# Performance work log

Measured on AMD Instinct MI355X. Metric: run time of the kernel, lower is better.

## Reference

```python
import jax, jax.numpy as jnp
import numpy as np

D_MODEL = 128
D_STATE = 16
D_CONV = 2
EXPAND = 2
D_INNER = EXPAND * D_MODEL  # 256
DT_RANK = (D_MODEL + 15) // 16  # 8
GROUPS = 4
EPS = 1e-5


def setup_inputs() -> dict:
    key = jax.random.key(0)
    ks = jax.random.split(key, 12)
    s = lambda k, shape, sc=0.02: jax.random.normal(k, shape, dtype=jnp.float32) * sc
    inp = {
        "x_hsi": jax.random.normal(ks[0], (8, D_MODEL, 64, 64), dtype=jnp.float32),
        "W_in": s(ks[1], (D_MODEL, 2 * D_INNER)),            # in_proj (no bias)
        "conv_w": s(ks[2], (D_INNER, D_CONV), 0.5),          # depthwise causal conv, k=2
        "conv_b": s(ks[3], (D_INNER,), 0.1),
        "W_x": s(ks[4], (D_INNER, DT_RANK + 2 * D_STATE)),   # x_proj (no bias)
        "W_dt": s(ks[5], (DT_RANK, D_INNER), 0.1),
        "b_dt": s(ks[6], (D_INNER,), 0.1),
        "A_log": jnp.log(jnp.broadcast_to(jnp.arange(1, D_STATE + 1, dtype=jnp.float32), (D_INNER, D_STATE))),
        "D": jnp.ones((D_INNER,), dtype=jnp.float32),
        "W_out": s(ks[7], (D_INNER, D_MODEL)),               # out_proj (no bias)
        "gn_gamma": jnp.ones((D_MODEL,), dtype=jnp.float32),
        "gn_beta": jnp.zeros((D_MODEL,), dtype=jnp.float32),
    }
    return inp


def _causal_conv_k2(x, w, b):
    # x: [B, L, Din]; w: [Din, 2]; causal depthwise conv, kernel size 2
    xp = jnp.pad(x, ((0, 0), (1, 0), (0, 0)))
    return xp[:, :-1] * w[:, 0] + xp[:, 1:] * w[:, 1] + b


def _selective_scan(xc, dt, Bmat, Cmat, A, D):
    # xc,dt: [B,L,Din]; Bmat,Cmat: [B,L,N]; A: [Din,N]; D: [Din]
    def step(h, inp):
        dt_t, B_t, C_t, x_t = inp          # [B,Din],[B,N],[B,N],[B,Din]
        dA = jnp.exp(dt_t[..., None] * A)                      # [B,Din,N]
        dBx = dt_t[..., None] * B_t[:, None, :] * x_t[..., None]
        h = dA * h + dBx
        y = jnp.einsum('bdn,bn->bd', h, C_t)
        return h, y

    B_, L, Din = xc.shape
    h0 = jnp.zeros((B_, Din, A.shape[1]), dtype=xc.dtype)
    xs = (jnp.swapaxes(dt, 0, 1), jnp.swapaxes(Bmat, 0, 1),
          jnp.swapaxes(Cmat, 0, 1), jnp.swapaxes(xc, 0, 1))
    _, ys = jax.lax.scan(step, h0, xs)     # ys: [L,B,Din]
    return jnp.swapaxes(ys, 0, 1) + xc * D


def _mamba(x, W_in, conv_w, conv_b, W_x, W_dt, b_dt, A_log, D, W_out):
    # x: [B, L, d_model]
    xz = x @ W_in                                   # [B,L,2*Din]
    xh, z = jnp.split(xz, 2, axis=-1)
    xh = jax.nn.silu(_causal_conv_k2(xh, conv_w, conv_b))
    x_dbl = xh @ W_x                                # [B,L,dt_rank+2N]
    dt_low = x_dbl[..., :DT_RANK]
    Bmat = x_dbl[..., DT_RANK:DT_RANK + D_STATE]
    Cmat = x_dbl[..., DT_RANK + D_STATE:]
    dt = jax.nn.softplus(dt_low @ W_dt + b_dt)      # [B,L,Din]
    A = -jnp.exp(A_log)
    y = _selective_scan(xh, dt, Bmat, Cmat, A, D)
    y = y * jax.nn.silu(z)
    return y @ W_out


def _group_norm(x, gamma, beta):
    # x: [B,C,H,W]
    B_, C, H, W = x.shape
    xr = x.reshape(B_, GROUPS, -1)
    mean = xr.mean(-1, keepdims=True)
    var = xr.var(-1, keepdims=True)
    xn = ((xr - mean) * jax.lax.rsqrt(var + EPS)).reshape(B_, C, H, W)
    return xn * gamma[:, None, None] + beta[:, None, None]


def reference(x_hsi, W_in, conv_w, conv_b, W_x, W_dt, b_dt, A_log, D, W_out, gn_gamma, gn_beta):
    B_, C, H, W = x_hsi.shape
    x = jnp.transpose(x_hsi, (0, 2, 3, 1)).reshape(B_, H * W, C)
    x = _mamba(x, W_in, conv_w, conv_b, W_x, W_dt, b_dt, A_log, D, W_out)
    x = jnp.transpose(x.reshape(B_, H, W, C), (0, 3, 1, 2))
    x = jax.nn.silu(_group_norm(x, gn_gamma, gn_beta))
    return x + x_hsi
```

## Files before the change

kernel.cpp:

```cpp
#include <hip/hip_runtime.h>
#include <hip/hip_bf16.h>
#include <hip/hip_fp16.h>
#include <math.h>

#define BATCH   8
#define LSEQ    4096
#define CMODEL  128
#define DIN     256
#define NSTATE  16
#define RRANK   8
#define NCH     128
#define TCH     32

typedef __attribute__((ext_vector_type(8))) short short8;
typedef __attribute__((ext_vector_type(4))) float f32x4;
typedef __attribute__((ext_vector_type(2))) float f32x2;

__device__ __forceinline__ float sigmoid_fast(float x) {
    return __builtin_amdgcn_rcpf(1.0f + __expf(-x));
}
__device__ __forceinline__ float silu_fast(float x) { return x * sigmoid_fast(x); }
__device__ __forceinline__ float softplus_fast(float x) {
    return fmaxf(x, 0.0f) + __logf(1.0f + __expf(-fabsf(x)));
}
__device__ __forceinline__ float bf2f(unsigned short u) {
    return __uint_as_float(((unsigned)u) << 16);
}
__device__ __forceinline__ unsigned pk2bf(float a, float b) {
    __hip_bfloat162 t = __float22bfloat162_rn(make_float2(a, b));
    unsigned r;
    __builtin_memcpy(&r, &t, 4);
    return r;
}
__device__ __forceinline__ unsigned short f2bf1(float v) {
    return (unsigned short)pk2bf(v, v);
}

__device__ __forceinline__ void dA_powers2(float dtv, const float* A, bool fast,
                                           f32x2* dA2)
{
    if (fast) {
        float e1 = __expf(dtv * A[0]);
        float e2 = e1 * e1;
        dA2[0] = (f32x2){e1, e2};
        f32x2 e2s = (f32x2){e2, e2};
        #pragma unroll
        for (int j = 1; j < 8; ++j) dA2[j] = dA2[j-1] * e2s;
    } else {
        #pragma unroll
        for (int j = 0; j < 8; ++j)
            dA2[j] = (f32x2){__expf(dtv * A[2*j]), __expf(dtv * A[2*j+1])};
    }
}

#define LSTR 72
#define YSTR 264

__device__ __forceinline__ void tr64_bf(const float* __restrict__ src, int lds,
                                        int r0, int c0,
                                        unsigned short* __restrict__ dst, int ldd)
{
    __shared__ float ts[64][65];
    const int tid = threadIdx.x;
    #pragma unroll
    for (int it = 0; it < 4; ++it) {
        int slot = tid + it * 256;
        int i = slot >> 4, j4 = slot & 15;
        float4 v = *(const float4*)&src[(size_t)(r0 + i) * lds + c0 + j4 * 4];
        ts[i][j4*4+0] = v.x; ts[i][j4*4+1] = v.y;
        ts[i][j4*4+2] = v.z; ts[i][j4*4+3] = v.w;
    }
    __syncthreads();
    #pragma unroll
    for (int it = 0; it < 4; ++it) {
        int slot = tid + it * 256;
        int row = slot >> 4, c4 = slot & 15;
        unsigned p0 = pk2bf(ts[c4*4+0][row], ts[c4*4+1][row]);
        unsigned p1 = pk2bf(ts[c4*4+2][row], ts[c4*4+3][row]);
        unsigned long long u = (unsigned long long)p0 | ((unsigned long long)p1 << 32);
        *(unsigned long long*)&dst[(size_t)(c0 + row) * ldd + r0 + c4 * 4] = u;
    }
}

__global__ __launch_bounds__(256) void k0_setup(
    const float* __restrict__ W_in, const float* __restrict__ W_out,
    const float* __restrict__ W_x,
    unsigned short* __restrict__ wtin, unsigned short* __restrict__ wtout,
    unsigned short* __restrict__ wxt, float* __restrict__ part)
{
    const int bid = blockIdx.x;
    if (bid < 16) {
        int ct = bid >> 3, jt = bid & 7;
        tr64_bf(W_in, 512, ct * 64, jt * 64, wtin, 128);
    } else if (bid < 24) {
        int t3 = bid - 16;
        int kt = t3 >> 1, ct = t3 & 1;
        tr64_bf(W_out, 128, kt * 64, ct * 64, wtout, 256);
    } else if (bid == 24) {
        for (int idx = threadIdx.x; idx < 48 * 256; idx += 256) {
            int j = idx >> 8, k = idx & 255;
            float v = (j < 40) ? W_x[k * 40 + j] : 0.0f;
            wxt[(size_t)j * 256 + k] = f2bf1(v);
        }
    } else {
        if (threadIdx.x < 64) part[threadIdx.x] = 0.0f;
    }
}

__global__ __launch_bounds__(512) void k1_gemm_in(
    const float* __restrict__ x_hsi, const unsigned short* __restrict__ wtin,
    unsigned short* __restrict__ xhbf, unsigned short* __restrict__ zbf)
{
    __shared__ __align__(16) unsigned short Abf[128 * LSTR];
    __shared__ __align__(16) unsigned short Bbf[256 * LSTR];
    const int tid = threadIdx.x;
    const int R0  = blockIdx.x * 128;
    const int b   = R0 >> 12;
    const int l0  = R0 & 4095;
    const int jbase = blockIdx.y * 256;

    const int w    = tid >> 6;
    const int lane = tid & 63;
    const int lm   = lane & 15;
    const int q    = lane >> 4;
    const int mbase = (w & 1) * 64;
    const int nbase = (w >> 1) * 64;

    f32x4 acc[4][4];
    #pragma unroll
    for (int i = 0; i < 4; ++i)
        #pragma unroll
        for (int j = 0; j < 4; ++j) acc[i][j] = (f32x4){0.f, 0.f, 0.f, 0.f};

    const int cq = tid & 15;
    const int lq = tid >> 4;

    for (int kc = 0; kc < 128; kc += 64) {
        __syncthreads();
        {
            float v[4][4];
            #pragma unroll
            for (int t = 0; t < 4; ++t) {
                float4 f = *(const float4*)&x_hsi[((b * 128 + kc + cq * 4 + t) << 12) + l0 + lq * 4];
                v[t][0] = f.x; v[t][1] = f.y; v[t][2] = f.z; v[t][3] = f.w;
            }
            #pragma unroll
            for (int i = 0; i < 4; ++i) {
                unsigned p0 = pk2bf(v[0][i], v[1][i]);
                unsigned p1 = pk2bf(v[2][i], v[3][i]);
                unsigned long long u = (unsigned long long)p0 | ((unsigned long long)p1 << 32);
                *(unsigned long long*)&Abf[(lq * 4 + i) * LSTR + cq * 4] = u;
            }
        }
        #pragma unroll
        for (int it = 0; it < 4; ++it) {
            int slot = tid + it * 512;
            int r = slot >> 3, seg = slot & 7;
            short8 vb = *(const short8*)&wtin[(size_t)(jbase + r) * 128 + kc + seg * 8];
            *(short8*)&Bbf[r * LSTR + seg * 8] = vb;
        }
        __syncthreads();
        #pragma unroll
        for (int kt = 0; kt < 2; ++kt) {
            short8 af[4], bfr[4];
            #pragma unroll
            for (int mt = 0; mt < 4; ++mt)
                af[mt] = *(const short8*)&Abf[(mbase + mt * 16 + lm) * LSTR + kt * 32 + q * 8];
            #pragma unroll
            for (int nt = 0; nt < 4; ++nt)
                bfr[nt] = *(const short8*)&Bbf[(nbase + nt * 16 + lm) * LSTR + kt * 32 + q * 8];
            #pragma unroll
            for (int mt = 0; mt < 4; ++mt)
                #pragma unroll
                for (int nt = 0; nt < 4; ++nt)
                    acc[mt][nt] = __builtin_amdgcn_mfma_f32_16x16x32_bf16(
                        af[mt], bfr[nt], acc[mt][nt], 0, 0, 0);
        }
    }

    const bool is_xh = (jbase == 0);
    #pragma unroll
    for (int mt = 0; mt < 4; ++mt) {
        #pragma unroll
        for (int r = 0; r < 4; ++r) {
            int row = R0 + mbase + mt * 16 + q * 4 + r;
            #pragma unroll
            for (int nt = 0; nt < 4; ++nt) {
                int col = nbase + nt * 16 + lm;
                float val = acc[mt][nt][r];
                if (is_xh) xhbf[row * 256 + col] = f2bf1(val);
                else       zbf[row * 256 + col]  = f2bf1(silu_fast(val));
            }
        }
    }
}

__global__ __launch_bounds__(256) void k46_conv_gemm_scan1(
    const unsigned short* __restrict__ xhbf, const float* __restrict__ conv_w,
    const float* __restrict__ conv_b, const unsigned short* __restrict__ wxt,
    const float* __restrict__ W_dt, const float* __restrict__ b_dt,
    const float* __restrict__ A_log,
    float* __restrict__ xdbl, unsigned short* __restrict__ xcbf,
    float* __restrict__ hend, float* __restrict__ dtsg)
{
    __shared__ float cw0[256], cw1[256], cbs[256];
    __shared__ __align__(16) unsigned short xcb[TCH][YSTR];
    __shared__ __align__(16) float xdl[TCH * 40];
    const int tid = threadIdx.x;
    const int chunk = blockIdx.x;
    const int b = blockIdx.y;
    const int R0 = b * LSEQ + chunk * TCH;

    cw0[tid] = conv_w[2 * tid];
    cw1[tid] = conv_w[2 * tid + 1];
    cbs[tid] = conv_b[tid];

    const int d = tid;
    float A[16];
    #pragma unroll
    for (int qq = 0; qq < 4; ++qq) {
        float4 al = *(const float4*)&A_log[d * 16 + qq * 4];
        A[qq*4+0] = -__expf(al.x); A[qq*4+1] = -__expf(al.y);
        A[qq*4+2] = -__expf(al.z); A[qq*4+3] = -__expf(al.w);
    }
    bool fast = true;
    #pragma unroll
    for (int n = 1; n < 16; ++n)
        fast = fast && (fabsf(A[n] - (n + 1) * A[0]) <= 1e-4f * fabsf(A[n]) + 1e-7f);
    float wdt[8];
    #pragma unroll
    for (int r = 0; r < 8; ++r) wdt[r] = W_dt[r * 256 + d];
    const float bdt = b_dt[d];

    __syncthreads();

    #pragma unroll
    for (int it = 0; it < 8; ++it) {
        int idx = tid + it * 256;
        int r = idx >> 6, qq = idx & 63;
        int row = R0 + r;
        int dd = qq * 4;
        ushort4 cu = *(const ushort4*)&xhbf[(size_t)row * 256 + dd];
        float cur[4] = {bf2f(cu.x), bf2f(cu.y), bf2f(cu.z), bf2f(cu.w)};
        float pv[4] = {0.f, 0.f, 0.f, 0.f};
        if ((row & 4095) != 0) {
            ushort4 pu = *(const ushort4*)&xhbf[(size_t)(row - 1) * 256 + dd];
            pv[0] = bf2f(pu.x); pv[1] = bf2f(pu.y);
            pv[2] = bf2f(pu.z); pv[3] = bf2f(pu.w);
        }
        float o[4];
        #pragma unroll
        for (int e = 0; e < 4; ++e)
            o[e] = silu_fast(pv[e] * cw0[dd+e] + cur[e] * cw1[dd+e] + cbs[dd+e]);
        unsigned p0 = pk2bf(o[0], o[1]), p1 = pk2bf(o[2], o[3]);
        unsigned long long u = (unsigned long long)p0 | ((unsigned long long)p1 << 32);
        *(unsigned long long*)&xcb[r][dd] = u;
        *(unsigned long long*)&xcbf[(size_t)row * 256 + dd] = u;
    }
    __syncthreads();

    const int w    = tid >> 6;
    const int lane = tid & 63;
    const int lm   = lane & 15;
    const int q    = lane >> 4;
    {
        const int mt  = w & 1;
        const int nlo = (w < 2) ? 0 : 2;
        const int nn  = (w < 2) ? 2 : 1;
        f32x4 macc[2];
        macc[0] = (f32x4){0.f,0.f,0.f,0.f};
        macc[1] = (f32x4){0.f,0.f,0.f,0.f};
        for (int kc = 0; kc < 256; kc += 32) {
            short8 af = *(const short8*)&xcb[mt * 16 + lm][kc + q * 8];
            #pragma unroll
            for (int t = 0; t < 2; ++t) {
                if (t < nn) {
                    short8 bfr = *(const short8*)&wxt[(size_t)((nlo + t) * 16 + lm) * 256 + kc + q * 8];
                    macc[t] = __builtin_amdgcn_mfma_f32_16x16x32_bf16(
                        af, bfr, macc[t], 0, 0, 0);
                }
            }
        }
        #pragma unroll
        for (int t = 0; t < 2; ++t) {
            if (t < nn) {
                #pragma unroll
                for (int r = 0; r < 4; ++r) {
                    int row = mt * 16 + q * 4 + r;
                    int col = (nlo + t) * 16 + lm;
                    if (col < 40) {
                        float v = macc[t][r];
                        xdl[row * 40 + col] = v;
                        xdbl[(size_t)(R0 + row) * 40 + col] = v;
                    }
                }
            }
        }
    }
    __syncthreads();

    f32x2 h2[8];
    #pragma unroll
    for (int j = 0; j < 8; ++j) h2[j] = (f32x2){0.f, 0.f};
    float dtsum = 0.f;

    #pragma unroll 2
    for (int tt = 0; tt < TCH; ++tt) {
        float xcv = bf2f(xcb[tt][d]);

        float dl[8];
        *(float4*)&dl[0] = *(const float4*)&xdl[tt * 40 + 0];
        *(float4*)&dl[4] = *(const float4*)&xdl[tt * 40 + 4];
        float dtr = bdt;
        #pragma unroll
        for (int r = 0; r < 8; ++r) dtr = fmaf(dl[r], wdt[r], dtr);
        float dtv = softplus_fast(dtr);
        dtsum += dtv;
        float dtx = dtv * xcv;

        float Bv[16];
        *(float4*)&Bv[0]  = *(const float4*)&xdl[tt * 40 + 8];
        *(float4*)&Bv[4]  = *(const float4*)&xdl[tt * 40 + 12];
        *(float4*)&Bv[8]  = *(const float4*)&xdl[tt * 40 + 16];
        *(float4*)&Bv[12] = *(const float4*)&xdl[tt * 40 + 20];

        f32x2 dA2[8];
        dA_powers2(dtv, A, fast, dA2);
        f32x2 dtx2 = (f32x2){dtx, dtx};
        #pragma unroll
        for (int j = 0; j < 8; ++j) {
            f32x2 Bt2 = (f32x2){Bv[2*j], Bv[2*j+1]};
            h2[j] = dA2[j] * h2[j] + dtx2 * Bt2;
        }
    }

    const float* hf = (const float*)h2;
    const int base = ((b * NCH + chunk) * 256 + d) * 16;
    #pragma unroll
    for (int qq = 0; qq < 4; ++qq)
        *(float4*)&hend[base + qq * 4] = make_float4(hf[qq*4], hf[qq*4+1], hf[qq*4+2], hf[qq*4+3]);
    dtsg[(b * NCH + chunk) * 256 + d] = dtsum;
}

__global__ __launch_bounds__(256) void k7_combine(
    const float* __restrict__ dtsg, const float* __restrict__ A_log,
    float* __restrict__ hx)
{
    const int idx = blockIdx.x * 256 + threadIdx.x;
    const int b = idx >> 12;
    const int rem = idx & 4095;
    const int d = rem >> 4, n = rem & 15;
    const float An = -__expf(A_log[d * 16 + n]);
    const int base = b * NCH * 4096 + rem;
    const int sbase = b * NCH * 256 + d;
    float h = 0.f;
    float Sb[8], Eb[8];
    #pragma unroll
    for (int j = 0; j < 8; ++j) {
        Sb[j] = dtsg[sbase + j * 256];
        Eb[j] = hx[base + j * 4096];
    }
    for (int g = 0; g < NCH / 8; ++g) {
        const int o  = base + g * 32768;
        const int so = sbase + g * 2048;
        float Sn[8] = {0,0,0,0,0,0,0,0}, En[8] = {0,0,0,0,0,0,0,0};
        if (g < NCH / 8 - 1) {
            #pragma unroll
            for (int j = 0; j < 8; ++j) {
                Sn[j] = dtsg[so + 2048 + j * 256];
                En[j] = hx[o + 32768 + j * 4096];
            }
        }
        #pragma unroll
        for (int j = 0; j < 8; ++j) {
            hx[o + j * 4096] = h;
            float P = __expf(Sb[j] * An);
            h = fmaf(P, h, Eb[j]);
        }
        #pragma unroll
        for (int j = 0; j < 8; ++j) { Sb[j] = Sn[j]; Eb[j] = En[j]; }
    }
}

__global__ __launch_bounds__(256) void k89_scan2_gemm_out(
    const unsigned short* __restrict__ xcbf, const float* __restrict__ xdbl,
    const float* __restrict__ W_dt, const float* __restrict__ b_dt,
    const float* __restrict__ A_log, const float* __restrict__ Dvec,
    const float* __restrict__ hin, const unsigned short* __restrict__ zbf,
    const unsigned short* __restrict__ wtout,
    unsigned short* __restrict__ out_bf, float* __restrict__ part)
{
    __shared__ __align__(16) unsigned short Ybf[TCH][YSTR];
    __shared__ float pred[8];
    const int tid = threadIdx.x;
    const int chunk = blockIdx.x;
    const int b = blockIdx.y;
    const int t0 = b * LSEQ + chunk * TCH;

    if (tid < 8) pred[tid] = 0.0f;

    const int d = tid;
    float A[16];
    #pragma unroll
    for (int qq = 0; qq < 4; ++qq) {
        float4 al = *(const float4*)&A_log[d * 16 + qq * 4];
        A[qq*4+0] = -__expf(al.x); A[qq*4+1] = -__expf(al.y);
        A[qq*4+2] = -__expf(al.z); A[qq*4+3] = -__expf(al.w);
    }
    bool fast = true;
    #pragma unroll
    for (int n = 1; n < 16; ++n)
        fast = fast && (fabsf(A[n] - (n + 1) * A[0]) <= 1e-4f * fabsf(A[n]) + 1e-7f);
    float wdt[8];
    #pragma unroll
    for (int r = 0; r < 8; ++r) wdt[r] = W_dt[r * 256 + d];
    const float bdt = b_dt[d];
    const float Dd = Dvec[d];

    f32x2 h2[8];
    {
        const int hbase = ((b * NCH + chunk) * 256 + d) * 16;
        float hf[16];
        #pragma unroll
        for (int qq = 0; qq < 4; ++qq) {
            float4 hv = *(const float4*)&hin[hbase + qq * 4];
            hf[qq*4+0] = hv.x; hf[qq*4+1] = hv.y; hf[qq*4+2] = hv.z; hf[qq*4+3] = hv.w;
        }
        #pragma unroll
        for (int j = 0; j < 8; ++j) h2[j] = (f32x2){hf[2*j], hf[2*j+1]};
    }

    #pragma unroll 2
    for (int tt = 0; tt < TCH; ++tt) {
        const int row = t0 + tt;
        const size_t gi = (size_t)row * 256 + d;
        float xcv = bf2f(xcbf[gi]);

        const float* xr = &xdbl[(size_t)row * 40];
        float dl[8], Bv[16], Cv[16];
        *(float4*)&dl[0] = *(const float4*)&xr[0];
        *(float4*)&dl[4] = *(const float4*)&xr[4];
        *(float4*)&Bv[0]  = *(const float4*)&xr[8];
        *(float4*)&Bv[4]  = *(const float4*)&xr[12];
        *(float4*)&Bv[8]  = *(const float4*)&xr[16];
        *(float4*)&Bv[12] = *(const float4*)&xr[20];
        *(float4*)&Cv[0]  = *(const float4*)&xr[24];
        *(float4*)&Cv[4]  = *(const float4*)&xr[28];
        *(float4*)&Cv[8]  = *(const float4*)&xr[32];
        *(float4*)&Cv[12] = *(const float4*)&xr[36];

        float dtr = bdt;
        #pragma unroll
        for (int r = 0; r < 8; ++r) dtr = fmaf(dl[r], wdt[r], dtr);
        float dtv = softplus_fast(dtr);
        float dtx = dtv * xcv;

        f32x2 dA2[8];
        dA_powers2(dtv, A, fast, dA2);
        f32x2 dtx2 = (f32x2){dtx, dtx};
        f32x2 yv2 = (f32x2){0.f, 0.f};
        #pragma unroll
        for (int j = 0; j < 8; ++j) {
            f32x2 Bt2 = (f32x2){Bv[2*j], Bv[2*j+1]};
            f32x2 Ct2 = (f32x2){Cv[2*j], Cv[2*j+1]};
            h2[j] = dA2[j] * h2[j] + dtx2 * Bt2;
            yv2 = yv2 + h2[j] * Ct2;
        }
        float yv = yv2.x + yv2.y;
        yv = fmaf(Dd, xcv, yv);
        Ybf[tt][d] = f2bf1(yv * bf2f(zbf[gi]));
    }
    __syncthreads();

    const int w    = tid >> 6;
    const int lane = tid & 63;
    const int lm   = lane & 15;
    const int q    = lane >> 4;
    const int mbase = (w & 1) * 64;
    const int nbase = (w >> 1) * 16;

    f32x4 acc[4];
    #pragma unroll
    for (int i = 0; i < 4; ++i) acc[i] = (f32x4){0.f, 0.f, 0.f, 0.f};

    for (int ks = 0; ks < 256; ks += 32) {
        short8 bfr = *(const short8*)&Ybf[nbase + lm][ks + q * 8];
        #pragma unroll
        for (int mt = 0; mt < 4; ++mt) {
            short8 af = *(const short8*)&wtout[(size_t)(mbase + mt * 16 + lm) * 256 + ks + q * 8];
            acc[mt] = __builtin_amdgcn_mfma_f32_16x16x32_bf16(
                af, bfr, acc[mt], 0, 0, 0);
        }
    }

    const int l0 = chunk * TCH;
    #pragma unroll
    for (int mt = 0; mt < 4; ++mt) {
        #pragma unroll
        for (int r = 0; r < 4; ++r) {
            int c = mbase + mt * 16 + q * 4 + r;
            long obase = (long)(b * 128 + c) * 4096 + l0;
            out_bf[obase + nbase + lm] = f2bf1(acc[mt][r]);
        }
    }

    float s0 = 0.f, q0 = 0.f, s1 = 0.f, q1 = 0.f;
    #pragma unroll
    for (int mt = 0; mt < 4; ++mt)
        #pragma unroll
        for (int r = 0; r < 4; ++r) {
            float v = acc[mt][r];
            if (mt < 2) { s0 += v; q0 += v * v; }
            else        { s1 += v; q1 += v * v; }
        }
    #pragma unroll
    for (int off = 32; off > 0; off >>= 1) {
        s0 += __shfl_down(s0, off, 64);
        q0 += __shfl_down(q0, off, 64);
        s1 += __shfl_down(s1, off, 64);
        q1 += __shfl_down(q1, off, 64);
    }
    if (lane == 0) {
        int g0 = mbase >> 5;
        atomicAdd(&pred[g0 * 2],           s0);
        atomicAdd(&pred[g0 * 2 + 1],       q0);
        atomicAdd(&pred[(g0 + 1) * 2],     s1);
        atomicAdd(&pred[(g0 + 1) * 2 + 1], q1);
    }
    __syncthreads();
    if (tid < 8) atomicAdd(&part[b * 8 + tid], pred[tid]);
}

__global__ __launch_bounds__(256) void k10c_apply(
    const unsigned short* __restrict__ out_bf, const float* __restrict__ part,
    const float* __restrict__ gamma, const float* __restrict__ beta,
    const float* __restrict__ x_hsi, float* __restrict__ out)
{
    __shared__ float sstat[64];
    if (threadIdx.x < 32) {
        float S = part[threadIdx.x * 2];
        float Q = part[threadIdx.x * 2 + 1];
        const float inv_n = 1.0f / 131072.0f;
        float mean = S * inv_n;
        float var  = Q * inv_n - mean * mean;
        sstat[threadIdx.x * 2]     = mean;
        sstat[threadIdx.x * 2 + 1] = rsqrtf(var + 1e-5f);
    }
    __syncthreads();
    const int idx4 = blockIdx.x * 256 + threadIdx.x;
    const int flat = idx4 * 4;
    const int c = (flat >> 12) & 127;
    const int b = flat >> 19;
    const int g = c >> 5;
    const float mean = sstat[(b * 4 + g) * 2];
    const float inv  = sstat[(b * 4 + g) * 2 + 1];
    const float ga = gamma[c], be = beta[c];
    ushort4 u = *(const ushort4*)&out_bf[flat];
    float4 r = *(const float4*)&x_hsi[flat];
    float vv[4] = {bf2f(u.x), bf2f(u.y), bf2f(u.z), bf2f(u.w)};
    float rr[4] = {r.x, r.y, r.z, r.w};
    float o[4];
    #pragma unroll
    for (int qq = 0; qq < 4; ++qq) {
        float xn = (vv[qq] - mean) * inv;
        float gv = xn * ga + be;
        o[qq] = silu_fast(gv) + rr[qq];
    }
    *(float4*)&out[flat] = make_float4(o[0], o[1], o[2], o[3]);
}

extern "C" void kernel_launch(void* const* d_in, const int* in_sizes, int n_in,
                              void* d_out, int out_size, void* d_ws, size_t ws_size,
                              hipStream_t stream)
{
    const float* x_hsi  = (const float*)d_in[0];
    const float* W_in   = (const float*)d_in[1];
    const float* conv_w = (const float*)d_in[2];
    const float* conv_b = (const float*)d_in[3];
    const float* W_x    = (const float*)d_in[4];
    const float* W_dt   = (const float*)d_in[5];
    const float* b_dt   = (const float*)d_in[6];
    const float* A_log  = (const float*)d_in[7];
    const float* Dv     = (const float*)d_in[8];
    const float* W_out  = (const float*)d_in[9];
    const float* gnw    = (const float*)d_in[10];
    const float* gnb    = (const float*)d_in[11];

    float* ws = (float*)d_ws;
    unsigned short* xhbf = (unsigned short*)(ws + 0);
    unsigned short* zbf  = (unsigned short*)(ws + 4194304);
    float* xdbl   = ws + 8388608;
    float* hx     = ws + 8716288;
    float* dtsg   = ws + 12910592;
    unsigned short* xcbf   = (unsigned short*)(ws + 13172736);
    unsigned short* out_bf = (unsigned short*)(ws + 17367040);
    float* part   = ws + 19464192;
    unsigned short* wtin  = (unsigned short*)(ws + 19464256);
    unsigned short* wtout = (unsigned short*)(ws + 19497024);
    unsigned short* wxt   = (unsigned short*)(ws + 19513408);
    float* outp   = (float*)d_out;

    k0_setup<<<26, 256, 0, stream>>>(W_in, W_out, W_x, wtin, wtout, wxt, part);
    k1_gemm_in<<<dim3(256, 2), 512, 0, stream>>>(x_hsi, wtin, xhbf, zbf);
    k46_conv_gemm_scan1<<<dim3(NCH, BATCH), 256, 0, stream>>>(
        xhbf, conv_w, conv_b, wxt, W_dt, b_dt, A_log, xdbl, xcbf, hx, dtsg);
    k7_combine<<<128, 256, 0, stream>>>(dtsg, A_log, hx);
    k89_scan2_gemm_out<<<dim3(NCH, BATCH), 256, 0, stream>>>(
        xcbf, xdbl, W_dt, b_dt, A_log, Dv, hx, zbf, wtout, out_bf, part);
    k10c_apply<<<4096, 256, 0, stream>>>(out_bf, part, gnw, gnb, x_hsi, outp);
}
```

Measured before the change: 192.1 us.

## Compute local scan output in first pass and apply decaying carry correction later

```diff
diff --git a/kernel.cpp b/kernel.cpp
--- a/kernel.cpp
+++ b/kernel.cpp
@@ -199,8 +199,8 @@
     const unsigned short* __restrict__ xhbf, const float* __restrict__ conv_w,
     const float* __restrict__ conv_b, const unsigned short* __restrict__ wxt,
     const float* __restrict__ W_dt, const float* __restrict__ b_dt,
-    const float* __restrict__ A_log,
-    float* __restrict__ xdbl, unsigned short* __restrict__ xcbf,
+    const float* __restrict__ A_log, const float* __restrict__ Dvec,
+    float* __restrict__ xdbl, __half* __restrict__ ylh,
     float* __restrict__ hend, float* __restrict__ dtsg)
 {
     __shared__ float cw0[256], cw1[256], cbs[256];
@@ -231,6 +231,7 @@
     #pragma unroll
     for (int r = 0; r < 8; ++r) wdt[r] = W_dt[r * 256 + d];
     const float bdt = b_dt[d];
+    const float Dd = Dvec[d];
 
     __syncthreads();
 
@@ -255,7 +256,6 @@
         unsigned p0 = pk2bf(o[0], o[1]), p1 = pk2bf(o[2], o[3]);
         unsigned long long u = (unsigned long long)p0 | ((unsigned long long)p1 << 32);
         *(unsigned long long*)&xcb[r][dd] = u;
-        *(unsigned long long*)&xcbf[(size_t)row * 256 + dd] = u;
     }
     __syncthreads();
 
@@ -318,20 +318,30 @@
         dtsum += dtv;
         float dtx = dtv * xcv;
 
-        float Bv[16];
+        float Bv[16], Cv[16];
         *(float4*)&Bv[0]  = *(const float4*)&xdl[tt * 40 + 8];
         *(float4*)&Bv[4]  = *(const float4*)&xdl[tt * 40 + 12];
         *(float4*)&Bv[8]  = *(const float4*)&xdl[tt * 40 + 16];
         *(float4*)&Bv[12] = *(const float4*)&xdl[tt * 40 + 20];
+        *(float4*)&Cv[0]  = *(const float4*)&xdl[tt * 40 + 24];
+        *(float4*)&Cv[4]  = *(const float4*)&xdl[tt * 40 + 28];
+        *(float4*)&Cv[8]  = *(const float4*)&xdl[tt * 40 + 32];
+        *(float4*)&Cv[12] = *(const float4*)&xdl[tt * 40 + 36];
 
         f32x2 dA2[8];
         dA_powers2(dtv, A, fast, dA2);
         f32x2 dtx2 = (f32x2){dtx, dtx};
+        f32x2 yv2 = (f32x2){0.f, 0.f};
         #pragma unroll
         for (int j = 0; j < 8; ++j) {
             f32x2 Bt2 = (f32x2){Bv[2*j], Bv[2*j+1]};
+            f32x2 Ct2 = (f32x2){Cv[2*j], Cv[2*j+1]};
             h2[j] = dA2[j] * h2[j] + dtx2 * Bt2;
-        }
+            yv2 = yv2 + h2[j] * Ct2;
+        }
+        float yv = yv2.x + yv2.y;
+        yv = fmaf(Dd, xcv, yv);
+        ylh[(size_t)(R0 + tt) * 256 + d] = __float2half(yv);
     }
 
     const float* hf = (const float*)h2;
@@ -382,11 +392,13 @@
     }
 }
 
-__global__ __launch_bounds__(256) void k89_scan2_gemm_out(
-    const unsigned short* __restrict__ xcbf, const float* __restrict__ xdbl,
+#define CORR_THR 10.0f
+
+__global__ __launch_bounds__(256) void k89_corr_gemm_out(
+    const __half* __restrict__ ylh, const float* __restrict__ xdbl,
     const float* __restrict__ W_dt, const float* __restrict__ b_dt,
-    const float* __restrict__ A_log, const float* __restrict__ Dvec,
-    const float* __restrict__ hin, const unsigned short* __restrict__ zbf,
+    const float* __restrict__ A_log, const float* __restrict__ hin,
+    const unsigned short* __restrict__ zbf,
     const unsigned short* __restrict__ wtout,
     unsigned short* __restrict__ out_bf, float* __restrict__ part)
 {
@@ -415,7 +427,7 @@
     #pragma unroll
     for (int r = 0; r < 8; ++r) wdt[r] = W_dt[r * 256 + d];
     const float bdt = b_dt[d];
-    const float Dd = Dvec[d];
+    const float negA0 = -A[0];
 
     f32x2 h2[8];
     {
@@ -430,20 +442,18 @@
         for (int j = 0; j < 8; ++j) h2[j] = (f32x2){hf[2*j], hf[2*j+1]};
     }
 
-    #pragma unroll 2
-    for (int tt = 0; tt < TCH; ++tt) {
+    const unsigned short* ylu = (const unsigned short*)ylh;
+
+    float cum = 0.f;
+    int tt = 0;
+    for (; tt < TCH; ++tt) {
         const int row = t0 + tt;
         const size_t gi = (size_t)row * 256 + d;
-        float xcv = bf2f(xcbf[gi]);
 
         const float* xr = &xdbl[(size_t)row * 40];
-        float dl[8], Bv[16], Cv[16];
+        float dl[8], Cv[16];
         *(float4*)&dl[0] = *(const float4*)&xr[0];
         *(float4*)&dl[4] = *(const float4*)&xr[4];
-        *(float4*)&Bv[0]  = *(const float4*)&xr[8];
-        *(float4*)&Bv[4]  = *(const float4*)&xr[12];
-        *(float4*)&Bv[8]  = *(const float4*)&xr[16];
-        *(float4*)&Bv[12] = *(const float4*)&xr[20];
         *(float4*)&Cv[0]  = *(const float4*)&xr[24];
         *(float4*)&Cv[4]  = *(const float4*)&xr[28];
         *(float4*)&Cv[8]  = *(const float4*)&xr[32];
@@ -452,23 +462,30 @@
         float dtr = bdt;
         #pragma unroll
         for (int r = 0; r < 8; ++r) dtr = fmaf(dl[r], wdt[r], dtr);
-        float dtv = softplus_fast(dtr);
-        float dtx = dtv * xcv;
-
-        f32x2 dA2[8];
-        dA_powers2(dtv, A, fast, dA2);
-        f32x2 dtx2 = (f32x2){dtx, dtx};
-        f32x2 yv2 = (f32x2){0.f, 0.f};
+        cum += softplus_fast(dtr);
+
+        f32x2 P2[8];
+        dA_powers2(cum, A, fast, P2);
+        f32x2 cr2 = (f32x2){0.f, 0.f};
         #pragma unroll
         for (int j = 0; j < 8; ++j) {
-            f32x2 Bt2 = (f32x2){Bv[2*j], Bv[2*j+1]};
             f32x2 Ct2 = (f32x2){Cv[2*j], Cv[2*j+1]};
-            h2[j] = dA2[j] * h2[j] + dtx2 * Bt2;
-            yv2 = yv2 + h2[j] * Ct2;
-        }
-        float yv = yv2.x + yv2.y;
-        yv = fmaf(Dd, xcv, yv);
-        Ybf[tt][d] = f2bf1(yv * bf2f(zbf[gi]));
+            cr2 = cr2 + Ct2 * (P2[j] * h2[j]);
+        }
+        unsigned short yu = ylu[gi];
+        __half yh;
+        __builtin_memcpy(&yh, &yu, 2);
+        float y = __half2float(yh) + cr2.x + cr2.y;
+        Ybf[tt][d] = f2bf1(y * bf2f(zbf[gi]));
+
+        if (__all(cum * negA0 > CORR_THR)) { ++tt; break; }
+    }
+    for (; tt < TCH; ++tt) {
+        const size_t gi = (size_t)(t0 + tt) * 256 + d;
+        unsigned short yu = ylu[gi];
+        __half yh;
+        __builtin_memcpy(&yh, &yu, 2);
+        Ybf[tt][d] = f2bf1(__half2float(yh) * bf2f(zbf[gi]));
     }
     __syncthreads();
 
@@ -592,7 +609,7 @@
     float* xdbl   = ws + 8388608;
     float* hx     = ws + 8716288;
     float* dtsg   = ws + 12910592;
-    unsigned short* xcbf   = (unsigned short*)(ws + 13172736);
+    __half* ylh   = (__half*)(ws + 13172736);
     unsigned short* out_bf = (unsigned short*)(ws + 17367040);
     float* part   = ws + 19464192;
     unsigned short* wtin  = (unsigned short*)(ws + 19464256);
@@ -603,9 +620,9 @@
     k0_setup<<<26, 256, 0, stream>>>(W_in, W_out, W_x, wtin, wtout, wxt, part);
     k1_gemm_in<<<dim3(256, 2), 512, 0, stream>>>(x_hsi, wtin, xhbf, zbf);
     k46_conv_gemm_scan1<<<dim3(NCH, BATCH), 256, 0, stream>>>(
-        xhbf, conv_w, conv_b, wxt, W_dt, b_dt, A_log, xdbl, xcbf, hx, dtsg);
+        xhbf, conv_w, conv_b, wxt, W_dt, b_dt, A_log, Dv, xdbl, ylh, hx, dtsg);
     k7_combine<<<128, 256, 0, stream>>>(dtsg, A_log, hx);
-    k89_scan2_gemm_out<<<dim3(NCH, BATCH), 256, 0, stream>>>(
-        xcbf, xdbl, W_dt, b_dt, A_log, Dv, hx, zbf, wtout, out_bf, part);
+    k89_corr_gemm_out<<<dim3(NCH, BATCH), 256, 0, stream>>>(
+        ylh, xdbl, W_dt, b_dt, A_log, hx, zbf, wtout, out_bf, part);
     k10c_apply<<<4096, 256, 0, stream>>>(out_bf, part, gnw, gnb, x_hsi, outp);
 }
```

Measured after the change: 190.2 us (median of 2 runs). No clear change (-1.0%).
